# Optimization experiments

Hardware: AMD Instinct MI355X
Metric: run time of the kernel (lower is better)

Reference implementation:

```python
import jax, jax.numpy as jnp
import numpy as np
import math

B, T = 64, 2000
RNN_DIM, EMB_DIM, ATT_DIM = 1024, 512, 128
STATIC_CH, STATIC_K = 8, 21
DYN_CH, DYN_K = 8, 21
PRIOR_LEN, ALPHA, BETA = 11, 0.1, 0.9


def _betabinom_pmf(k, n, a, b):
    lg = math.lgamma
    return math.exp(lg(n + 1) - lg(k + 1) - lg(n - k + 1)
                    + lg(k + a) + lg(n - k + b) - lg(n + a + b)
                    - (lg(a) + lg(b) - lg(a + b)))


def setup_inputs() -> dict:
    key = jax.random.key(0)
    ks = jax.random.split(key, 12)
    query = jax.random.normal(ks[0], (B, RNN_DIM), jnp.float32)
    memory = jax.random.normal(ks[1], (B, T, EMB_DIM), jnp.float32)
    a = jax.random.uniform(ks[2], (B, T), jnp.float32)
    alignment_pre = a / jnp.sum(a, axis=1, keepdims=True)  # valid attention distribution
    mask = jnp.zeros((B, T), dtype=bool)
    s = 1.0 / math.sqrt(RNN_DIM)
    W_w = jax.random.uniform(ks[3], (ATT_DIM, RNN_DIM), jnp.float32, -s, s)
    W_b = jax.random.uniform(ks[4], (ATT_DIM,), jnp.float32, -s, s)
    V_w = jax.random.normal(ks[5], (DYN_CH * DYN_K, ATT_DIM), jnp.float32) * 0.05
    F_w = jax.random.normal(ks[6], (STATIC_CH, 1, STATIC_K), jnp.float32) * 0.1
    U_w = jax.random.normal(ks[7], (ATT_DIM, STATIC_CH), jnp.float32) * 0.1
    T_w = jax.random.normal(ks[8], (ATT_DIM, DYN_CH), jnp.float32) * 0.1
    T_b = jax.random.normal(ks[9], (ATT_DIM,), jnp.float32) * 0.05
    v_w = jax.random.normal(ks[10], (1, ATT_DIM), jnp.float32) * 0.1
    P_np = np.array([_betabinom_pmf(k, PRIOR_LEN - 1, ALPHA, BETA) for k in range(PRIOR_LEN)], np.float32)
    P = jnp.asarray(P_np[::-1].copy())  # buffer: flipped beta-binomial prior
    return {"attention_hidden_state": query, "memory": memory, "alignment_pre": alignment_pre,
            "mask": mask, "W_w": W_w, "W_b": W_b, "V_w": V_w, "F_w": F_w,
            "U_w": U_w, "T_w": T_w, "T_b": T_b, "v_w": v_w, "P": P}


def _conv1d(lhs, rhs, pad, groups=1):
    # lhs [N,C,T], rhs [O,C//groups,K]; cross-correlation, matching torch conv1d
    return jax.lax.conv_general_dilated(lhs, rhs, (1,), [pad],
                                        dimension_numbers=("NCH", "OIH", "NCH"),
                                        feature_group_count=groups)


def reference(attention_hidden_state, memory, alignment_pre, mask,
              W_w, W_b, V_w, F_w, U_w, T_w, T_b, v_w, P):
    b, t = alignment_pre.shape
    # log of causal beta-binomial prior: left-pad by prior_length-1, valid conv
    p = _conv1d(alignment_pre[:, None, :], P.reshape(1, 1, -1), (PRIOR_LEN - 1, 0))[:, 0, :]
    p = jnp.log(jnp.clip(p, 1e-6))
    # per-sample dynamic kernels: [B, dyn_ch*K]
    G = jnp.tanh(attention_hidden_state @ W_w.T + W_b) @ V_w.T
    g = _conv1d(alignment_pre[None, :, :], G.reshape(b * DYN_CH, 1, DYN_K),
                ((DYN_K - 1) // 2, (DYN_K - 1) // 2), groups=b)  # [1, B*dyn_ch, T]
    g = g.reshape(b, DYN_CH, t).transpose(0, 2, 1)  # [B, T, dyn_ch]
    # static conv features
    f = _conv1d(alignment_pre[:, None, :], F_w,
                ((STATIC_K - 1) // 2, (STATIC_K - 1) // 2)).transpose(0, 2, 1)  # [B, T, static_ch]
    e = (jnp.tanh(f @ U_w.T + g @ T_w.T + T_b) @ v_w.T)[..., 0] + p  # [B, T]
    e = jnp.where(mask, -jnp.inf, e)
    attention_weights = jax.nn.softmax(e, axis=1)
    attention_context = jnp.einsum("bt,bte->be", attention_weights, memory)
    return attention_context, attention_weights
```

## Files before the change

### kernel.cpp

```cpp
#include <hip/hip_runtime.h>

#define B_   64
#define T_   2000
#define RNN_ 1024
#define EMB_ 512
#define ATT_ 128
#define CH_  8
#define K_   21
#define PL_  11
#define GSZ  168
#define CCHK 64
#define NCC  32

typedef float vf4 __attribute__((ext_vector_type(4)));

__device__ __forceinline__ float fast_tanh(float x) {
    float ax = fabsf(x);
    float e  = __expf(2.0f * ax);
    float t  = 1.0f - 2.0f / (e + 1.0f);
    return copysignf(t, x);
}

__global__ __launch_bounds__(256) void k_gen_dyn(
    const float* __restrict__ q, const float* __restrict__ Ww,
    const float* __restrict__ Wb, const float* __restrict__ Vw,
    float* __restrict__ G, float* __restrict__ out_ctx)
{
    __shared__ float sq[RNN_];
    __shared__ float part[256];
    __shared__ float sh[ATT_];
    const int b = blockIdx.x, tid = threadIdx.x;
    for (int i = tid; i < EMB_; i += 256) out_ctx[b * EMB_ + i] = 0.f;
    for (int i = tid; i < RNN_; i += 256) sq[i] = q[b * RNN_ + i];
    __syncthreads();
    {
        const int row = tid & 127, half = tid >> 7;
        const float4* wr = reinterpret_cast<const float4*>(Ww + row * RNN_ + half * (RNN_ / 2));
        const float4* qr = reinterpret_cast<const float4*>(sq + half * (RNN_ / 2));
        float acc = 0.f;
        #pragma unroll 8
        for (int i = 0; i < RNN_ / 8; ++i) {
            float4 w4 = wr[i], q4 = qr[i];
            acc += w4.x * q4.x + w4.y * q4.y + w4.z * q4.z + w4.w * q4.w;
        }
        part[tid] = acc;
    }
    __syncthreads();
    if (tid < ATT_) sh[tid] = fast_tanh(part[tid] + part[tid + 128] + Wb[tid]);
    __syncthreads();
    for (int o = tid; o < GSZ; o += 256) {
        const float4* vr = reinterpret_cast<const float4*>(Vw + o * ATT_);
        const float4* hr = reinterpret_cast<const float4*>(sh);
        float acc = 0.f;
        #pragma unroll 8
        for (int i = 0; i < ATT_ / 4; ++i) {
            float4 v4 = vr[i], h4 = hr[i];
            acc += v4.x * h4.x + v4.y * h4.y + v4.z * h4.z + v4.w * h4.w;
        }
        G[b * GSZ + o] = acc;
    }
}

__global__ __launch_bounds__(256, 4) void k_eng_stream(
    const float* __restrict__ a,  const float* __restrict__ G,
    const float* __restrict__ Fw, const float* __restrict__ Uw,
    const float* __restrict__ Tw, const float* __restrict__ Tb,
    const float* __restrict__ vw, const float* __restrict__ P,
    const unsigned char* __restrict__ mask, const float* __restrict__ mem,
    float* __restrict__ pws, float* __restrict__ sred,
    float* __restrict__ out_ctx)
{
    __shared__ union {
        struct {
            float FG[K_ * 16];
            float UT[ATT_ * 16];
            float Tb[ATT_]; float V[ATT_]; float Pr[PL_];
            float Q[4 * CCHK]; float red[4];
        } E;
        struct { vf4 part[2][EMB_ / 4]; } C;
    } sm;
    __shared__ float sA[CCHK + K_ - 1];
    __shared__ float sp[CCHK];

    const int b = blockIdx.x, c = blockIdx.y, tid = threadIdx.x;
    const int t0 = c * CCHK;
    const int nvalid = min(CCHK, T_ - t0);
    const int tloc = tid & (CCHK - 1);
    const int qq = tid >> 6;

    for (int j = tid; j < CCHK + K_ - 1; j += 256) {
        int idx = t0 - 10 + j;
        sA[j] = (idx >= 0 && idx < T_) ? a[b * T_ + idx] : 0.f;
    }
    for (int j = tid; j < 2 * GSZ; j += 256) {
        if (j < GSZ) sm.E.FG[(j % K_) * 16 + (j / K_)] = Fw[j];
        else { int jj = j - GSZ; sm.E.FG[(jj % K_) * 16 + 8 + (jj / K_)] = G[b * GSZ + jj]; }
    }
    for (int j = tid; j < ATT_ * CH_; j += 256) {
        int d = j >> 3, ch = j & 7;
        sm.E.UT[d * 16 + ch]     = Uw[j];
        sm.E.UT[d * 16 + 8 + ch] = Tw[j];
    }
    if (tid < ATT_) { sm.E.Tb[tid] = Tb[tid]; sm.E.V[tid] = vw[tid]; }
    if (tid < PL_)  sm.E.Pr[tid] = P[tid];
    __syncthreads();

    {
        float fg[16];
        #pragma unroll
        for (int i = 0; i < 16; ++i) fg[i] = 0.f;
        #pragma unroll
        for (int k = 0; k < K_; ++k) {
            float av = sA[tloc + k];
            const vf4* fp = reinterpret_cast<const vf4*>(&sm.E.FG[k * 16]);
            vf4 x0 = fp[0], x1 = fp[1], x2 = fp[2], x3 = fp[3];
            fg[0]  += x0.x * av; fg[1]  += x0.y * av; fg[2]  += x0.z * av; fg[3]  += x0.w * av;
            fg[4]  += x1.x * av; fg[5]  += x1.y * av; fg[6]  += x1.z * av; fg[7]  += x1.w * av;
            fg[8]  += x2.x * av; fg[9]  += x2.y * av; fg[10] += x2.z * av; fg[11] += x2.w * av;
            fg[12] += x3.x * av; fg[13] += x3.y * av; fg[14] += x3.z * av; fg[15] += x3.w * av;
        }
        float accQ = 0.f;
        const int d0 = qq * 32;
        #pragma unroll 4
        for (int dd = 0; dd < 32; ++dd) {
            const int d = d0 + dd;
            const vf4* up = reinterpret_cast<const vf4*>(&sm.E.UT[d * 16]);
            vf4 u0 = up[0], u1 = up[1], u2 = up[2], u3 = up[3];
            float s0 = u0.x * fg[0]  + u0.y * fg[1]  + u0.z * fg[2]  + u0.w * fg[3];
            float s1 = u1.x * fg[4]  + u1.y * fg[5]  + u1.z * fg[6]  + u1.w * fg[7];
            float s2 = u2.x * fg[8]  + u2.y * fg[9]  + u2.z * fg[10] + u2.w * fg[11];
            float s3 = u3.x * fg[12] + u3.y * fg[13] + u3.z * fg[14] + u3.w * fg[15];
            float s = (sm.E.Tb[d] + s0) + (s1 + s2) + s3;
            accQ += sm.E.V[d] * fast_tanh(s);
        }
        sm.E.Q[qq * CCHK + tloc] = accQ;
    }
    __syncthreads();

    float pv = 0.f;
    if (tid < CCHK) {
        const int t = t0 + tid;
        if (t < T_ && !mask[b * T_ + min(t, T_ - 1)]) {
            float pp = 0.f;
            #pragma unroll
            for (int k = 0; k < PL_; ++k) pp += sm.E.Pr[k] * sA[tid + k];
            float e = (sm.E.Q[tid] + sm.E.Q[CCHK + tid])
                    + (sm.E.Q[2 * CCHK + tid] + sm.E.Q[3 * CCHK + tid])
                    + __logf(fmaxf(pp, 1e-6f));
            pv = __expf(e);
        }
        sp[tid] = pv;
        if (t0 + tid < T_) pws[b * T_ + t0 + tid] = pv;
    }
    float ssum = pv;
    #pragma unroll
    for (int off = 32; off > 0; off >>= 1) ssum += __shfl_xor(ssum, off);
    if ((tid & 63) == 0) sm.E.red[tid >> 6] = ssum;
    __syncthreads();
    if (tid == 0)
        sred[b * NCC + c] = sm.E.red[0] + sm.E.red[1] + sm.E.red[2] + sm.E.red[3];
    __syncthreads();

    {
        const int col = tid & 127, rp = tid >> 7;
        const float* basep = mem + ((size_t)(b * T_ + t0)) * EMB_ + col * 4;
        vf4 acc0 = {0.f, 0.f, 0.f, 0.f}, acc1 = {0.f, 0.f, 0.f, 0.f};
        if (nvalid == CCHK) {
            #pragma unroll
            for (int i = 0; i < CCHK / 4; ++i) {
                const int r0 = rp + 4 * i, r1 = rp + 4 * i + 2;
                vf4 m0 = *reinterpret_cast<const vf4*>(basep + (size_t)r0 * EMB_);
                vf4 m1 = *reinterpret_cast<const vf4*>(basep + (size_t)r1 * EMB_);
                acc0 += sp[r0] * m0;
                acc1 += sp[r1] * m1;
            }
        } else {
            for (int tt = rp; tt < nvalid; tt += 2) {
                vf4 mv = *reinterpret_cast<const vf4*>(basep + (size_t)tt * EMB_);
                acc0 += sp[tt] * mv;
            }
        }
        sm.C.part[rp][col] = acc0 + acc1;
    }
    __syncthreads();
    if (tid < 128) {
        vf4 r = sm.C.part[0][tid];
        r += sm.C.part[1][tid];
        float* op = out_ctx + b * EMB_ + tid * 4;
        atomicAdd(op + 0, r.x); atomicAdd(op + 1, r.y);
        atomicAdd(op + 2, r.z); atomicAdd(op + 3, r.w);
    }
}

__global__ __launch_bounds__(256) void k_final(
    const float* __restrict__ sred, const float* __restrict__ pws,
    float* __restrict__ out_ctx, float* __restrict__ out_w)
{
    __shared__ float sS;
    const int b = blockIdx.x, tid = threadIdx.x;
    float v = (tid < NCC) ? sred[b * NCC + tid] : 0.f;
    #pragma unroll
    for (int off = 16; off > 0; off >>= 1) v += __shfl_xor(v, off);
    if (tid == 0) sS = v;
    __syncthreads();
    const float inv = 1.0f / sS;
    for (int i = tid; i < EMB_; i += 256) out_ctx[b * EMB_ + i] *= inv;
    for (int j = tid; j < T_; j += 256) out_w[b * T_ + j] = pws[b * T_ + j] * inv;
}

extern "C" void kernel_launch(void* const* d_in, const int* in_sizes, int n_in,
                              void* d_out, int out_size, void* d_ws, size_t ws_size,
                              hipStream_t stream)
{
    const float* q    = (const float*)d_in[0];
    const float* mem  = (const float*)d_in[1];
    const float* a    = (const float*)d_in[2];
    const unsigned char* mask = (const unsigned char*)d_in[3];
    const float* Ww = (const float*)d_in[4];
    const float* Wb = (const float*)d_in[5];
    const float* Vw = (const float*)d_in[6];
    const float* Fw = (const float*)d_in[7];
    const float* Uw = (const float*)d_in[8];
    const float* Tw = (const float*)d_in[9];
    const float* Tb = (const float*)d_in[10];
    const float* vw = (const float*)d_in[11];
    const float* P  = (const float*)d_in[12];

    float* out_ctx = (float*)d_out;
    float* out_w   = out_ctx + B_ * EMB_;

    float* G    = (float*)d_ws;
    float* sred = G + B_ * GSZ;
    float* pws  = sred + B_ * NCC;

    k_gen_dyn<<<B_, 256, 0, stream>>>(q, Ww, Wb, Vw, G, out_ctx);
    k_eng_stream<<<dim3(B_, NCC), 256, 0, stream>>>(a, G, Fw, Uw, Tw, Tb, vw, P,
                                                    mask, mem, pws, sred, out_ctx);
    k_final<<<B_, 256, 0, stream>>>(sred, pws, out_ctx, out_w);
}
```

Measured before the change: 85.12 us.

## Fuse final normalization into streaming kernel via last-block atomic counter

Removes the separate k_final launch. Each (batch, chunk) block bumps a per-batch atomic counter, and the last block to finish sums the partial softmax denominators and normalizes the context and weights for that batch. Stores of partial sums and unnormalized weights become atomics so the last block sees them coherently, and the counter is reset in the first kernel. This saves one launch and its tail, at the cost of atomic traffic and a serialized normalization pass in 64 tail blocks.

After: 159.3 us. 1.87x slower.

```diff
diff --git a/kernel.cpp b/kernel.cpp
--- a/kernel.cpp
+++ b/kernel.cpp
@@ -24,12 +24,14 @@
 __global__ __launch_bounds__(256) void k_gen_dyn(
     const float* __restrict__ q, const float* __restrict__ Ww,
     const float* __restrict__ Wb, const float* __restrict__ Vw,
-    float* __restrict__ G, float* __restrict__ out_ctx)
+    float* __restrict__ G, float* __restrict__ out_ctx,
+    unsigned* __restrict__ cnt)
 {
     __shared__ float sq[RNN_];
     __shared__ float part[256];
     __shared__ float sh[ATT_];
     const int b = blockIdx.x, tid = threadIdx.x;
+    if (tid == 0) cnt[b] = 0u;
     for (int i = tid; i < EMB_; i += 256) out_ctx[b * EMB_ + i] = 0.f;
     for (int i = tid; i < RNN_; i += 256) sq[i] = q[b * RNN_ + i];
     __syncthreads();
@@ -68,7 +70,8 @@
     const float* __restrict__ vw, const float* __restrict__ P,
     const unsigned char* __restrict__ mask, const float* __restrict__ mem,
     float* __restrict__ pws, float* __restrict__ sred,
-    float* __restrict__ out_ctx)
+    unsigned* __restrict__ cnt,
+    float* __restrict__ out_ctx, float* __restrict__ out_w)
 {
     __shared__ union {
         struct {
@@ -81,6 +84,8 @@
     } sm;
     __shared__ float sA[CCHK + K_ - 1];
     __shared__ float sp[CCHK];
+    __shared__ unsigned sLast;
+    __shared__ float sS;
 
     const int b = blockIdx.x, c = blockIdx.y, tid = threadIdx.x;
     const int t0 = c * CCHK;
@@ -150,7 +155,7 @@
             pv = __expf(e);
         }
         sp[tid] = pv;
-        if (t0 + tid < T_) pws[b * T_ + t0 + tid] = pv;
+        if (t0 + tid < T_) atomicExch(&pws[b * T_ + t0 + tid], pv);
     }
     float ssum = pv;
     #pragma unroll
@@ -158,7 +163,8 @@
     if ((tid & 63) == 0) sm.E.red[tid >> 6] = ssum;
     __syncthreads();
     if (tid == 0)
-        sred[b * NCC + c] = sm.E.red[0] + sm.E.red[1] + sm.E.red[2] + sm.E.red[3];
+        atomicExch(&sred[b * NCC + c],
+                   sm.E.red[0] + sm.E.red[1] + sm.E.red[2] + sm.E.red[3]);
     __syncthreads();
 
     {
@@ -190,22 +196,32 @@
         atomicAdd(op + 0, r.x); atomicAdd(op + 1, r.y);
         atomicAdd(op + 2, r.z); atomicAdd(op + 3, r.w);
     }
-}
-
-__global__ __launch_bounds__(256) void k_final(
-    const float* __restrict__ sred, const float* __restrict__ pws,
-    float* __restrict__ out_ctx, float* __restrict__ out_w)
-{
-    __shared__ float sS;
-    const int b = blockIdx.x, tid = threadIdx.x;
-    float v = (tid < NCC) ? sred[b * NCC + tid] : 0.f;
-    #pragma unroll
-    for (int off = 16; off > 0; off >>= 1) v += __shfl_xor(v, off);
-    if (tid == 0) sS = v;
-    __syncthreads();
-    const float inv = 1.0f / sS;
-    for (int i = tid; i < EMB_; i += 256) out_ctx[b * EMB_ + i] *= inv;
-    for (int j = tid; j < T_; j += 256) out_w[b * T_ + j] = pws[b * T_ + j] * inv;
+    __syncthreads();
+
+    if (tid == 0) {
+        __threadfence();
+        unsigned old = atomicAdd(&cnt[b], 1u);
+        sLast = (old == NCC - 1) ? 1u : 0u;
+    }
+    __syncthreads();
+    if (sLast) {
+        if (tid == 0) {
+            float S = 0.f;
+            #pragma unroll
+            for (int i = 0; i < NCC; ++i) S += atomicAdd(&sred[b * NCC + i], 0.f);
+            sS = S;
+        }
+        __syncthreads();
+        const float inv = 1.0f / sS;
+        for (int i = tid; i < EMB_; i += 256) {
+            float v = atomicAdd(&out_ctx[b * EMB_ + i], 0.f);
+            out_ctx[b * EMB_ + i] = v * inv;
+        }
+        for (int j = tid; j < T_; j += 256) {
+            float p = atomicAdd(&pws[b * T_ + j], 0.f);
+            out_w[b * T_ + j] = p * inv;
+        }
+    }
 }
 
 extern "C" void kernel_launch(void* const* d_in, const int* in_sizes, int n_in,
@@ -229,12 +245,13 @@
     float* out_ctx = (float*)d_out;
     float* out_w   = out_ctx + B_ * EMB_;
 
-    float* G    = (float*)d_ws;
-    float* sred = G + B_ * GSZ;
-    float* pws  = sred + B_ * NCC;
-
-    k_gen_dyn<<<B_, 256, 0, stream>>>(q, Ww, Wb, Vw, G, out_ctx);
+    float* G      = (float*)d_ws;
+    float* sred   = G + B_ * GSZ;
+    float* pws    = sred + B_ * NCC;
+    unsigned* cnt = (unsigned*)(pws + B_ * T_);
+
+    k_gen_dyn<<<B_, 256, 0, stream>>>(q, Ww, Wb, Vw, G, out_ctx, cnt);
     k_eng_stream<<<dim3(B_, NCC), 256, 0, stream>>>(a, G, Fw, Uw, Tw, Tb, vw, P,
-                                                    mask, mem, pws, sred, out_ctx);
-    k_final<<<B_, 256, 0, stream>>>(sred, pws, out_ctx, out_w);
-}
+                                                    mask, mem, pws, sred, cnt,
+                                                    out_ctx, out_w);
+}
```

## Fuse dynamic-kernel generation into streaming kernel and replace atomics with partial buffers

Applied to the files above, without the earlier changes.

The separate per-batch kernel that computes the dynamic conv filters is removed. Each of the 32 chunk blocks per batch now recomputes tanh(Wq+b) and V·h itself before the energy computation, which saves one launch and the serialization between the first two kernels. The cost is that the 128x1024 matvec runs 32 times redundantly per batch, reading Ww from L2 each time. Context accumulation switches from global atomicAdd to per-chunk partial stores, which the final kernel reduces, so out_ctx no longer needs to be zeroed beforehand.

New measurement: 166.3 us. 95.4% more time.

```diff
diff --git a/kernel.cpp b/kernel.cpp
--- a/kernel.cpp
+++ b/kernel.cpp
@@ -21,56 +21,19 @@
     return copysignf(t, x);
 }
 
-__global__ __launch_bounds__(256) void k_gen_dyn(
-    const float* __restrict__ q, const float* __restrict__ Ww,
-    const float* __restrict__ Wb, const float* __restrict__ Vw,
-    float* __restrict__ G, float* __restrict__ out_ctx)
-{
-    __shared__ float sq[RNN_];
-    __shared__ float part[256];
-    __shared__ float sh[ATT_];
-    const int b = blockIdx.x, tid = threadIdx.x;
-    for (int i = tid; i < EMB_; i += 256) out_ctx[b * EMB_ + i] = 0.f;
-    for (int i = tid; i < RNN_; i += 256) sq[i] = q[b * RNN_ + i];
-    __syncthreads();
-    {
-        const int row = tid & 127, half = tid >> 7;
-        const float4* wr = reinterpret_cast<const float4*>(Ww + row * RNN_ + half * (RNN_ / 2));
-        const float4* qr = reinterpret_cast<const float4*>(sq + half * (RNN_ / 2));
-        float acc = 0.f;
-        #pragma unroll 8
-        for (int i = 0; i < RNN_ / 8; ++i) {
-            float4 w4 = wr[i], q4 = qr[i];
-            acc += w4.x * q4.x + w4.y * q4.y + w4.z * q4.z + w4.w * q4.w;
-        }
-        part[tid] = acc;
-    }
-    __syncthreads();
-    if (tid < ATT_) sh[tid] = fast_tanh(part[tid] + part[tid + 128] + Wb[tid]);
-    __syncthreads();
-    for (int o = tid; o < GSZ; o += 256) {
-        const float4* vr = reinterpret_cast<const float4*>(Vw + o * ATT_);
-        const float4* hr = reinterpret_cast<const float4*>(sh);
-        float acc = 0.f;
-        #pragma unroll 8
-        for (int i = 0; i < ATT_ / 4; ++i) {
-            float4 v4 = vr[i], h4 = hr[i];
-            acc += v4.x * h4.x + v4.y * h4.y + v4.z * h4.z + v4.w * h4.w;
-        }
-        G[b * GSZ + o] = acc;
-    }
-}
-
-__global__ __launch_bounds__(256, 4) void k_eng_stream(
-    const float* __restrict__ a,  const float* __restrict__ G,
-    const float* __restrict__ Fw, const float* __restrict__ Uw,
-    const float* __restrict__ Tw, const float* __restrict__ Tb,
-    const float* __restrict__ vw, const float* __restrict__ P,
-    const unsigned char* __restrict__ mask, const float* __restrict__ mem,
+__global__ __launch_bounds__(256, 4) void k_fused(
+    const float* __restrict__ q,   const float* __restrict__ mem,
+    const float* __restrict__ a,   const unsigned char* __restrict__ mask,
+    const float* __restrict__ Ww,  const float* __restrict__ Wb,
+    const float* __restrict__ Vw,  const float* __restrict__ Fw,
+    const float* __restrict__ Uw,  const float* __restrict__ Tw,
+    const float* __restrict__ Tb,  const float* __restrict__ vw,
+    const float* __restrict__ P,
     float* __restrict__ pws, float* __restrict__ sred,
-    float* __restrict__ out_ctx)
+    float* __restrict__ ctxp)
 {
     __shared__ union {
+        struct { float qbuf[RNN_]; float part[256]; } A;
         struct {
             float FG[K_ * 16];
             float UT[ATT_ * 16];
@@ -79,6 +42,7 @@
         } E;
         struct { vf4 part[2][EMB_ / 4]; } C;
     } sm;
+    __shared__ float sh_[ATT_];
     __shared__ float sA[CCHK + K_ - 1];
     __shared__ float sp[CCHK];
 
@@ -88,13 +52,32 @@
     const int tloc = tid & (CCHK - 1);
     const int qq = tid >> 6;
 
+    for (int i = tid; i < RNN_ / 4; i += 256)
+        reinterpret_cast<vf4*>(sm.A.qbuf)[i] =
+            reinterpret_cast<const vf4*>(q + b * RNN_)[i];
     for (int j = tid; j < CCHK + K_ - 1; j += 256) {
         int idx = t0 - 10 + j;
         sA[j] = (idx >= 0 && idx < T_) ? a[b * T_ + idx] : 0.f;
     }
-    for (int j = tid; j < 2 * GSZ; j += 256) {
-        if (j < GSZ) sm.E.FG[(j % K_) * 16 + (j / K_)] = Fw[j];
-        else { int jj = j - GSZ; sm.E.FG[(jj % K_) * 16 + 8 + (jj / K_)] = G[b * GSZ + jj]; }
+    __syncthreads();
+    {
+        const int row = tid & 127, half = tid >> 7;
+        const vf4* wr = reinterpret_cast<const vf4*>(Ww + row * RNN_ + half * (RNN_ / 2));
+        const vf4* qr = reinterpret_cast<const vf4*>(sm.A.qbuf + half * (RNN_ / 2));
+        float acc = 0.f;
+        #pragma unroll 8
+        for (int i = 0; i < RNN_ / 8; ++i) {
+            vf4 w4 = wr[i], q4 = qr[i];
+            acc += w4.x * q4.x + w4.y * q4.y + w4.z * q4.z + w4.w * q4.w;
+        }
+        sm.A.part[tid] = acc;
+    }
+    __syncthreads();
+    if (tid < ATT_) sh_[tid] = fast_tanh(sm.A.part[tid] + sm.A.part[tid + 128] + Wb[tid]);
+    __syncthreads();
+
+    for (int j = tid; j < GSZ; j += 256) {
+        sm.E.FG[(j % K_) * 16 + (j / K_)] = Fw[j];
     }
     for (int j = tid; j < ATT_ * CH_; j += 256) {
         int d = j >> 3, ch = j & 7;
@@ -103,6 +86,17 @@
     }
     if (tid < ATT_) { sm.E.Tb[tid] = Tb[tid]; sm.E.V[tid] = vw[tid]; }
     if (tid < PL_)  sm.E.Pr[tid] = P[tid];
+    if (tid < GSZ) {
+        const vf4* vr = reinterpret_cast<const vf4*>(Vw + tid * ATT_);
+        const vf4* hr = reinterpret_cast<const vf4*>(sh_);
+        float acc = 0.f;
+        #pragma unroll 8
+        for (int i = 0; i < ATT_ / 4; ++i) {
+            vf4 v4 = vr[i], h4 = hr[i];
+            acc += v4.x * h4.x + v4.y * h4.y + v4.z * h4.z + v4.w * h4.w;
+        }
+        sm.E.FG[(tid % K_) * 16 + 8 + (tid / K_)] = acc;
+    }
     __syncthreads();
 
     {
@@ -186,14 +180,13 @@
     if (tid < 128) {
         vf4 r = sm.C.part[0][tid];
         r += sm.C.part[1][tid];
-        float* op = out_ctx + b * EMB_ + tid * 4;
-        atomicAdd(op + 0, r.x); atomicAdd(op + 1, r.y);
-        atomicAdd(op + 2, r.z); atomicAdd(op + 3, r.w);
+        reinterpret_cast<vf4*>(ctxp + ((size_t)(b * NCC + c)) * EMB_)[tid] = r;
     }
 }
 
 __global__ __launch_bounds__(256) void k_final(
     const float* __restrict__ sred, const float* __restrict__ pws,
+    const float* __restrict__ ctxp,
     float* __restrict__ out_ctx, float* __restrict__ out_w)
 {
     __shared__ float sS;
@@ -204,7 +197,13 @@
     if (tid == 0) sS = v;
     __syncthreads();
     const float inv = 1.0f / sS;
-    for (int i = tid; i < EMB_; i += 256) out_ctx[b * EMB_ + i] *= inv;
+    if (tid < EMB_ / 4) {
+        const vf4* cp = reinterpret_cast<const vf4*>(ctxp + (size_t)b * NCC * EMB_) + tid;
+        vf4 acc = {0.f, 0.f, 0.f, 0.f};
+        #pragma unroll
+        for (int i = 0; i < NCC; ++i) acc += cp[i * (EMB_ / 4)];
+        reinterpret_cast<vf4*>(out_ctx + b * EMB_)[tid] = acc * inv;
+    }
     for (int j = tid; j < T_; j += 256) out_w[b * T_ + j] = pws[b * T_ + j] * inv;
 }
 
@@ -229,12 +228,12 @@
     float* out_ctx = (float*)d_out;
     float* out_w   = out_ctx + B_ * EMB_;
 
-    float* G    = (float*)d_ws;
-    float* sred = G + B_ * GSZ;
+    float* sred = (float*)d_ws;
     float* pws  = sred + B_ * NCC;
-
-    k_gen_dyn<<<B_, 256, 0, stream>>>(q, Ww, Wb, Vw, G, out_ctx);
-    k_eng_stream<<<dim3(B_, NCC), 256, 0, stream>>>(a, G, Fw, Uw, Tw, Tb, vw, P,
-                                                    mask, mem, pws, sred, out_ctx);
-    k_final<<<B_, 256, 0, stream>>>(sred, pws, out_ctx, out_w);
-}
+    float* ctxp = pws + B_ * T_;
+
+    k_fused<<<dim3(B_, NCC), 256, 0, stream>>>(q, mem, a, mask, Ww, Wb, Vw, Fw,
+                                               Uw, Tw, Tb, vw, P,
+                                               pws, sred, ctxp);
+    k_final<<<B_, 256, 0, stream>>>(sred, pws, ctxp, out_ctx, out_w);
+}
```
